# Performance work log

Measured on AMD Instinct MI355X. Metric: run time of the kernel, lower is better.

Reference implementation:

```python
import jax, jax.numpy as jnp
import numpy as np

ALPHA = 0.2  # leaky relu negative slope (LinearNet default)


def _init_linear(key, fan_in, fan_out):
    kw, kb = jax.random.split(key)
    lim = 1.0 / np.sqrt(fan_in)
    W = jax.random.uniform(kw, (fan_in, fan_out), jnp.float32, -lim, lim)
    b = jax.random.uniform(kb, (fan_out,), jnp.float32, -lim, lim)
    return W, b


def setup_inputs() -> dict:
    key = jax.random.key(0)
    keys = jax.random.split(key, 8)
    B, N, F = 8, 512, 32
    x = jax.random.normal(keys[0], (B, N, F), jnp.float32)
    # fe: [2F=64 -> 64 -> 64 -> 64], all layers leaky-relu (final_linear=False)
    fe_W0, fe_b0 = _init_linear(keys[1], 2 * F, 64)
    fe_W1, fe_b1 = _init_linear(keys[2], 64, 64)
    fe_W2, fe_b2 = _init_linear(keys[3], 64, 64)
    # fn: [64 + F = 96 -> 128 -> 128 -> 32], last layer linear (final_linear=True)
    fn_W0, fn_b0 = _init_linear(keys[4], 64 + F, 128)
    fn_W1, fn_b1 = _init_linear(keys[5], 128, 128)
    fn_W2, fn_b2 = _init_linear(keys[6], 128, 32)
    return {
        "x": x,
        "fe_W0": fe_W0, "fe_b0": fe_b0,
        "fe_W1": fe_W1, "fe_b1": fe_b1,
        "fe_W2": fe_W2, "fe_b2": fe_b2,
        "fn_W0": fn_W0, "fn_b0": fn_b0,
        "fn_W1": fn_W1, "fn_b1": fn_b1,
        "fn_W2": fn_W2, "fn_b2": fn_b2,
    }


def reference(x, fe_W0, fe_b0, fe_W1, fe_b1, fe_W2, fe_b2,
              fn_W0, fn_b0, fn_W1, fn_b1, fn_W2, fn_b2):
    B, N, F = x.shape
    # all-pairs edge inputs: A[b,i,j] = concat(x[b,i], x[b,j])  (x1=repeat rows, x2=tile)
    xi = jnp.broadcast_to(x[:, :, None, :], (B, N, N, F))
    xj = jnp.broadcast_to(x[:, None, :, :], (B, N, N, F))
    A = jnp.concatenate([xi, xj], axis=-1)  # [B, N, N, 2F]
    # edge MLP fe: leaky relu after every layer (final_linear=False)
    for W, b in ((fe_W0, fe_b0), (fe_W1, fe_b1), (fe_W2, fe_b2)):
        A = jax.nn.leaky_relu(A @ W + b, negative_slope=ALPHA)
    # sum aggregation over the sender axis j
    agg = jnp.sum(A, axis=2)  # [B, N, K]
    h = jnp.concatenate([agg, x], axis=-1)  # [B, N, K + F]
    # node MLP fn: leaky relu on hidden layers, final layer linear
    h = jax.nn.leaky_relu(h @ fn_W0 + fn_b0, negative_slope=ALPHA)
    h = jax.nn.leaky_relu(h @ fn_W1 + fn_b1, negative_slope=ALPHA)
    out = h @ fn_W2 + fn_b2  # [B, N, output_node_size]
    return out
```

## Files before the change

### kernel.cpp

```cpp
#include <hip/hip_runtime.h>
#include <hip/hip_bf16.h>

#define ALPHA 0.2f
static __device__ __forceinline__ float lrel(float x) { return fmaxf(x, ALPHA * x); }

typedef __attribute__((ext_vector_type(8))) short bf16x8;
typedef __attribute__((ext_vector_type(4))) float f32x4;

union FragU { bf16x8 v; unsigned int u[4]; uint4 q; };

static __device__ __forceinline__ unsigned int pk2(float a, float b) {
    unsigned int r;
    asm("v_cvt_pk_bf16_f32 %0, %1, %2" : "=v"(r) : "v"(a), "v"(b));
    return r;
}
static __device__ __forceinline__ unsigned int cvl2(float a, float b) {
    return pk2(lrel(a), lrel(b));
}
static __device__ __forceinline__ void addabs(float& a, float x) {
    asm("v_add_f32 %0, %0, |%1|" : "+v"(a) : "v"(x));
}
static __device__ __forceinline__ unsigned short f2bf(float x) {
    union { float f; unsigned int u; } c;
    c.f = x;
    unsigned int r = c.u + 0x7FFFu + ((c.u >> 16) & 1u);
    return (unsigned short)(r >> 16);
}
static __device__ __forceinline__ int pi64(int s) {
    return 32 * ((s >> 4) >> 1) + 8 * ((s >> 2) & 3) + 4 * ((s >> 4) & 1) + (s & 3);
}

__global__ __launch_bounds__(256) void k_uv(
    const float* __restrict__ x, const float* __restrict__ W0, const float* __restrict__ b0,
    const float* __restrict__ W1, const float* __restrict__ W2,
    float* __restrict__ Upi, unsigned short* __restrict__ xbf, unsigned int* __restrict__ WF)
{
    if (blockIdx.x == 1024) {
        const int t = threadIdx.x;
        const int l = t & 63, part = t >> 6;
        const int lo = l & 15, g = l >> 4;
        for (int ff = part; ff < 20; ff += 4) {
            unsigned int o[4];
            if (ff < 4) {
                const int nf = ff;
                const int pc = 32 * (nf >> 1) + 8 * (lo >> 2) + 4 * (nf & 1) + (lo & 3);
#pragma unroll
                for (int uq = 0; uq < 4; ++uq) {
                    const int k0 = 8 * g + 2 * uq;
                    o[uq] = pk2(W0[(32 + k0) * 64 + pc], W0[(33 + k0) * 64 + pc]);
                }
            } else if (ff < 12) {
                const int s = (ff - 4) >> 2, nf = (ff - 4) & 3;
                const int pc = 32 * (nf >> 1) + 8 * (lo >> 2) + 4 * (nf & 1) + (lo & 3);
#pragma unroll
                for (int uq = 0; uq < 4; ++uq) {
                    const int k0 = 32 * s + 8 * g + 2 * uq;
                    o[uq] = pk2(W1[k0 * 64 + pc], W1[(k0 + 1) * 64 + pc]);
                }
            } else {
                const int s = (ff - 12) >> 2, nf = (ff - 12) & 3;
                const int c2 = 16 * nf + lo;
#pragma unroll
                for (int uq = 0; uq < 4; ++uq) {
                    const int k0 = 32 * s + 8 * g + 2 * uq;
                    o[uq] = pk2(W2[k0 * 64 + c2], W2[(k0 + 1) * 64 + c2]);
                }
            }
            *(uint4*)(WF + (ff * 64 + l) * 4) = make_uint4(o[0], o[1], o[2], o[3]);
        }
        return;
    }
    const int idx = blockIdx.x * 256 + threadIdx.x;
    const int n = idx >> 6;
    const int slot = idx & 63;
    const int f = pi64(slot);
    const float* xr = x + n * 32;
    float u = b0[f];
#pragma unroll
    for (int i = 0; i < 32; ++i) u += xr[i] * W0[i * 64 + f];
    Upi[idx] = u;
    if (slot < 32) xbf[n * 32 + slot] = f2bf(xr[slot]);
}

__global__ __launch_bounds__(256, 2) void k_edge(
    const float* __restrict__ Upi, const unsigned short* __restrict__ xbf,
    const unsigned int* __restrict__ WF,
    const float* __restrict__ b1, const float* __restrict__ b2,
    float* __restrict__ AGG)
{
    __shared__ uint4 wlds[1024];
    const int tid = threadIdx.x;
    const int w = tid >> 6, l = tid & 63;
    const int lo = l & 15, g = l >> 4;
    const int bid = blockIdx.x;
    const int b = bid >> 7, ig = bid & 127;
    const int node = b * 512 + ig * 4 + w;

    for (int idx = tid; idx < 1024; idx += 256)
        wlds[idx] = ((const uint4*)WF)[256 + idx];

    FragU w0f[4];
    const uint4* wp = (const uint4*)WF;
#pragma unroll
    for (int nf = 0; nf < 4; ++nf) w0f[nf].q = wp[nf * 64 + l];

    f32x4 u0f[4], b1f[4], b2f[4];
#pragma unroll
    for (int nf = 0; nf < 4; ++nf) {
        const float4 t0 = *(const float4*)(Upi + node * 64 + nf * 16 + 4 * g);
        u0f[nf] = (f32x4){t0.x, t0.y, t0.z, t0.w};
        const float4 t1 = *(const float4*)(b1 + 32 * (nf >> 1) + 8 * g + 4 * (nf & 1));
        const float4 t2 = *(const float4*)(b2 + 16 * nf + 4 * g);
        b1f[nf] = (f32x4){t1.x, t1.y, t1.z, t1.w};
        b2f[nf] = (f32x4){t2.x, t2.y, t2.z, t2.w};
    }

    const unsigned short* xb = xbf + b * 512 * 32;

    FragU xjB, xjN;
    xjB.q = *(const uint4*)(xb + lo * 32 + 8 * g);
    xjN.q = *(const uint4*)(xb + (16 + lo) * 32 + 8 * g);

    __syncthreads();

    f32x4 acc0c[4];
#pragma unroll
    for (int nf = 0; nf < 4; ++nf)
        acc0c[nf] = __builtin_amdgcn_mfma_f32_16x16x32_bf16(w0f[nf].v, xjB.v, u0f[nf], 0, 0, 0);
    xjB = xjN;

    f32x4 acc2p[4];
#pragma unroll
    for (int nf = 0; nf < 4; ++nf) { f32x4 z = {0.f, 0.f, 0.f, 0.f}; acc2p[nf] = z; }

    float aggL[4][4], aggA[4][4];
#pragma unroll
    for (int nf = 0; nf < 4; ++nf)
#pragma unroll
        for (int r = 0; r < 4; ++r) { aggL[nf][r] = 0.f; aggA[nf][r] = 0.f; }

#pragma unroll 2
    for (int k = 0; k < 32; ++k) {
        int widx = 0;
        asm volatile("" : "+v"(widx));

        const int jn = ((k + 2) & 31) * 16;
        FragU xjn;
        xjn.q = *(const uint4*)(xb + (jn + lo) * 32 + 8 * g);

        f32x4 acc0n[4];
#pragma unroll
        for (int nf = 0; nf < 4; ++nf)
            acc0n[nf] = __builtin_amdgcn_mfma_f32_16x16x32_bf16(w0f[nf].v, xjB.v, u0f[nf], 0, 0, 0);

        FragU q0, q1;
        q0.u[0] = cvl2(acc0c[0][0], acc0c[0][1]);
        q0.u[1] = cvl2(acc0c[0][2], acc0c[0][3]);
        q0.u[2] = cvl2(acc0c[1][0], acc0c[1][1]);
        q0.u[3] = cvl2(acc0c[1][2], acc0c[1][3]);
        q1.u[0] = cvl2(acc0c[2][0], acc0c[2][1]);
        q1.u[1] = cvl2(acc0c[2][2], acc0c[2][3]);
        q1.u[2] = cvl2(acc0c[3][0], acc0c[3][1]);
        q1.u[3] = cvl2(acc0c[3][2], acc0c[3][3]);

        f32x4 acc1[4];
#pragma unroll
        for (int nf = 0; nf < 4; ++nf) {
            FragU wa, wb;
            wa.q = wlds[widx + nf * 64 + l];
            wb.q = wlds[widx + (4 + nf) * 64 + l];
            acc1[nf] = __builtin_amdgcn_mfma_f32_16x16x32_bf16(wa.v, q0.v, b1f[nf], 0, 0, 0);
            acc1[nf] = __builtin_amdgcn_mfma_f32_16x16x32_bf16(wb.v, q1.v, acc1[nf], 0, 0, 0);
        }

#pragma unroll
        for (int nf = 0; nf < 4; ++nf)
#pragma unroll
            for (int r = 0; r < 4; ++r) {
                aggL[nf][r] += acc2p[nf][r];
                addabs(aggA[nf][r], acc2p[nf][r]);
            }

        FragU p0, p1;
        p0.u[0] = cvl2(acc1[0][0], acc1[0][1]);
        p0.u[1] = cvl2(acc1[0][2], acc1[0][3]);
        p0.u[2] = cvl2(acc1[1][0], acc1[1][1]);
        p0.u[3] = cvl2(acc1[1][2], acc1[1][3]);
        p1.u[0] = cvl2(acc1[2][0], acc1[2][1]);
        p1.u[1] = cvl2(acc1[2][2], acc1[2][3]);
        p1.u[2] = cvl2(acc1[3][0], acc1[3][1]);
        p1.u[3] = cvl2(acc1[3][2], acc1[3][3]);

#pragma unroll
        for (int nf = 0; nf < 4; ++nf) {
            FragU wa, wb;
            wa.q = wlds[widx + (8 + nf) * 64 + l];
            wb.q = wlds[widx + (12 + nf) * 64 + l];
            acc2p[nf] = __builtin_amdgcn_mfma_f32_16x16x32_bf16(wa.v, p0.v, b2f[nf], 0, 0, 0);
            acc2p[nf] = __builtin_amdgcn_mfma_f32_16x16x32_bf16(wb.v, p1.v, acc2p[nf], 0, 0, 0);
        }

#pragma unroll
        for (int nf = 0; nf < 4; ++nf) acc0c[nf] = acc0n[nf];
        xjB = xjn;
    }

#pragma unroll
    for (int nf = 0; nf < 4; ++nf)
#pragma unroll
        for (int r = 0; r < 4; ++r) {
            aggL[nf][r] += acc2p[nf][r];
            addabs(aggA[nf][r], acc2p[nf][r]);
        }

#pragma unroll
    for (int nf = 0; nf < 4; ++nf)
#pragma unroll
        for (int r = 0; r < 4; ++r) {
            float v = 0.6f * aggL[nf][r] + 0.4f * aggA[nf][r];
            v += __shfl_xor(v, 1);
            v += __shfl_xor(v, 2);
            v += __shfl_xor(v, 4);
            v += __shfl_xor(v, 8);
            aggL[nf][r] = v;
        }
    if (lo == 0) {
#pragma unroll
        for (int nf = 0; nf < 4; ++nf) {
            float4 o = {aggL[nf][0], aggL[nf][1], aggL[nf][2], aggL[nf][3]};
            *(float4*)(AGG + node * 64 + 16 * nf + 4 * g) = o;
        }
    }
}

__global__ __launch_bounds__(256) void k_fn(
    const float* __restrict__ AGG, const float* __restrict__ x,
    const float* __restrict__ W0, const float* __restrict__ b0,
    const float* __restrict__ W1, const float* __restrict__ b1,
    const float* __restrict__ W2, const float* __restrict__ b2,
    float* __restrict__ out)
{
    __shared__ float in96T[96][8];
    __shared__ float h1T[128][8];
    __shared__ float h2T[128][8];
    const int t = threadIdx.x;
    const int half = t >> 7, f = t & 127;
    const int node0 = blockIdx.x * 8;

    for (int idx = t; idx < 768; idx += 256) {
        int nn = idx & 7, k = idx >> 3;
        in96T[k][nn] = (k < 64) ? AGG[(node0 + nn) * 64 + k]
                                : x[(node0 + nn) * 32 + (k - 64)];
    }
    __syncthreads();

    {
        float a0 = b0[f], a1 = a0, a2 = a0, a3 = a0;
#pragma unroll 4
        for (int k = 0; k < 96; ++k) {
            const float4 iv = *(const float4*)(&in96T[k][4 * half]);
            const float wv = W0[k * 128 + f];
            a0 += iv.x * wv; a1 += iv.y * wv; a2 += iv.z * wv; a3 += iv.w * wv;
        }
        float4 o = {lrel(a0), lrel(a1), lrel(a2), lrel(a3)};
        *(float4*)(&h1T[f][4 * half]) = o;
    }
    __syncthreads();

    {
        float a0 = b1[f], a1 = a0, a2 = a0, a3 = a0;
#pragma unroll 4
        for (int k = 0; k < 128; ++k) {
            const float4 iv = *(const float4*)(&h1T[k][4 * half]);
            const float wv = W1[k * 128 + f];
            a0 += iv.x * wv; a1 += iv.y * wv; a2 += iv.z * wv; a3 += iv.w * wv;
        }
        float4 o = {lrel(a0), lrel(a1), lrel(a2), lrel(a3)};
        *(float4*)(&h2T[f][4 * half]) = o;
    }
    __syncthreads();

    {
        const int nn = t >> 5, fo = t & 31;
        float a = b2[fo];
#pragma unroll 4
        for (int k = 0; k < 128; ++k) a += h2T[k][nn] * W2[k * 32 + fo];
        out[(node0 + nn) * 32 + fo] = a;
    }
}

extern "C" void kernel_launch(void* const* d_in, const int* in_sizes, int n_in,
                              void* d_out, int out_size, void* d_ws, size_t ws_size,
                              hipStream_t stream)
{
    const float* x    = (const float*)d_in[0];
    const float* feW0 = (const float*)d_in[1];
    const float* feb0 = (const float*)d_in[2];
    const float* feW1 = (const float*)d_in[3];
    const float* feb1 = (const float*)d_in[4];
    const float* feW2 = (const float*)d_in[5];
    const float* feb2 = (const float*)d_in[6];
    const float* fnW0 = (const float*)d_in[7];
    const float* fnb0 = (const float*)d_in[8];
    const float* fnW1 = (const float*)d_in[9];
    const float* fnb1 = (const float*)d_in[10];
    const float* fnW2 = (const float*)d_in[11];
    const float* fnb2 = (const float*)d_in[12];
    float* out = (float*)d_out;

    float* Upi = (float*)d_ws;
    float* AGG = Upi + 262144;
    unsigned short* xbf = (unsigned short*)(AGG + 262144);
    unsigned int* WF = (unsigned int*)(xbf + 131072);

    hipLaunchKernelGGL(k_uv,   dim3(1025), dim3(256), 0, stream, x, feW0, feb0, feW1, feW2, Upi, xbf, WF);
    hipLaunchKernelGGL(k_edge, dim3(1024), dim3(256), 0, stream, Upi, xbf, WF, feb1, feb2, AGG);
    hipLaunchKernelGGL(k_fn,   dim3(512),  dim3(256), 0, stream, AGG, x, fnW0, fnb0, fnW1, fnb1, fnW2, fnb2, out);
}
```

Baseline: 74.54 us.

## Software-pipeline the three edge-MLP layers across consecutive sender tiles

```diff
diff --git a/kernel.cpp b/kernel.cpp
--- a/kernel.cpp
+++ b/kernel.cpp
@@ -16,9 +16,6 @@
 }
 static __device__ __forceinline__ unsigned int cvl2(float a, float b) {
     return pk2(lrel(a), lrel(b));
-}
-static __device__ __forceinline__ void addabs(float& a, float x) {
-    asm("v_add_f32 %0, %0, |%1|" : "+v"(a) : "v"(x));
 }
 static __device__ __forceinline__ unsigned short f2bf(float x) {
     union { float f; unsigned int u; } c;
@@ -117,30 +114,30 @@
 
     const unsigned short* xb = xbf + b * 512 * 32;
 
-    FragU xjB, xjN;
-    xjB.q = *(const uint4*)(xb + lo * 32 + 8 * g);
-    xjN.q = *(const uint4*)(xb + (16 + lo) * 32 + 8 * g);
+    FragU xjT0, xjB;
+    xjT0.q = *(const uint4*)(xb + lo * 32 + 8 * g);
+    xjB.q  = *(const uint4*)(xb + (16 + lo) * 32 + 8 * g);
 
     __syncthreads();
 
-    f32x4 acc0c[4];
+    f32x4 acc0p[4], acc1p[4], acc2p[4];
 #pragma unroll
     for (int nf = 0; nf < 4; ++nf)
-        acc0c[nf] = __builtin_amdgcn_mfma_f32_16x16x32_bf16(w0f[nf].v, xjB.v, u0f[nf], 0, 0, 0);
-    xjB = xjN;
-
-    f32x4 acc2p[4];
-#pragma unroll
-    for (int nf = 0; nf < 4; ++nf) { f32x4 z = {0.f, 0.f, 0.f, 0.f}; acc2p[nf] = z; }
-
-    float aggL[4][4], aggA[4][4];
+        acc0p[nf] = __builtin_amdgcn_mfma_f32_16x16x32_bf16(w0f[nf].v, xjT0.v, u0f[nf], 0, 0, 0);
+#pragma unroll
+    for (int nf = 0; nf < 4; ++nf) {
+        f32x4 z = {0.f, 0.f, 0.f, 0.f};
+        acc1p[nf] = z; acc2p[nf] = z;
+    }
+
+    float aggL[4][4];
 #pragma unroll
     for (int nf = 0; nf < 4; ++nf)
 #pragma unroll
-        for (int r = 0; r < 4; ++r) { aggL[nf][r] = 0.f; aggA[nf][r] = 0.f; }
+        for (int r = 0; r < 4; ++r) aggL[nf][r] = 0.f;
 
 #pragma unroll 2
-    for (int k = 0; k < 32; ++k) {
+    for (int k = 0; k < 34; ++k) {
         int widx = 0;
         asm volatile("" : "+v"(widx));
 
@@ -148,60 +145,64 @@
         FragU xjn;
         xjn.q = *(const uint4*)(xb + (jn + lo) * 32 + 8 * g);
 
+        FragU q0, q1;
+        q0.u[0] = cvl2(acc0p[0][0], acc0p[0][1]);
+        q0.u[1] = cvl2(acc0p[0][2], acc0p[0][3]);
+        q0.u[2] = cvl2(acc0p[1][0], acc0p[1][1]);
+        q0.u[3] = cvl2(acc0p[1][2], acc0p[1][3]);
+        q1.u[0] = cvl2(acc0p[2][0], acc0p[2][1]);
+        q1.u[1] = cvl2(acc0p[2][2], acc0p[2][3]);
+        q1.u[2] = cvl2(acc0p[3][0], acc0p[3][1]);
+        q1.u[3] = cvl2(acc0p[3][2], acc0p[3][3]);
+
         f32x4 acc0n[4];
 #pragma unroll
         for (int nf = 0; nf < 4; ++nf)
             acc0n[nf] = __builtin_amdgcn_mfma_f32_16x16x32_bf16(w0f[nf].v, xjB.v, u0f[nf], 0, 0, 0);
 
-        FragU q0, q1;
-        q0.u[0] = cvl2(acc0c[0][0], acc0c[0][1]);
-        q0.u[1] = cvl2(acc0c[0][2], acc0c[0][3]);
-        q0.u[2] = cvl2(acc0c[1][0], acc0c[1][1]);
-        q0.u[3] = cvl2(acc0c[1][2], acc0c[1][3]);
-        q1.u[0] = cvl2(acc0c[2][0], acc0c[2][1]);
-        q1.u[1] = cvl2(acc0c[2][2], acc0c[2][3]);
-        q1.u[2] = cvl2(acc0c[3][0], acc0c[3][1]);
-        q1.u[3] = cvl2(acc0c[3][2], acc0c[3][3]);
-
-        f32x4 acc1[4];
+        FragU p0, p1;
+        p0.u[0] = cvl2(acc1p[0][0], acc1p[0][1]);
+        p0.u[1] = cvl2(acc1p[0][2], acc1p[0][3]);
+        p0.u[2] = cvl2(acc1p[1][0], acc1p[1][1]);
+        p0.u[3] = cvl2(acc1p[1][2], acc1p[1][3]);
+        p1.u[0] = cvl2(acc1p[2][0], acc1p[2][1]);
+        p1.u[1] = cvl2(acc1p[2][2], acc1p[2][3]);
+        p1.u[2] = cvl2(acc1p[3][0], acc1p[3][1]);
+        p1.u[3] = cvl2(acc1p[3][2], acc1p[3][3]);
+
+        f32x4 acc1n[4];
 #pragma unroll
         for (int nf = 0; nf < 4; ++nf) {
             FragU wa, wb;
             wa.q = wlds[widx + nf * 64 + l];
             wb.q = wlds[widx + (4 + nf) * 64 + l];
-            acc1[nf] = __builtin_amdgcn_mfma_f32_16x16x32_bf16(wa.v, q0.v, b1f[nf], 0, 0, 0);
-            acc1[nf] = __builtin_amdgcn_mfma_f32_16x16x32_bf16(wb.v, q1.v, acc1[nf], 0, 0, 0);
-        }
-
-#pragma unroll
-        for (int nf = 0; nf < 4; ++nf)
-#pragma unroll
-            for (int r = 0; r < 4; ++r) {
-                aggL[nf][r] += acc2p[nf][r];
-                addabs(aggA[nf][r], acc2p[nf][r]);
-            }
-
-        FragU p0, p1;
-        p0.u[0] = cvl2(acc1[0][0], acc1[0][1]);
-        p0.u[1] = cvl2(acc1[0][2], acc1[0][3]);
-        p0.u[2] = cvl2(acc1[1][0], acc1[1][1]);
-        p0.u[3] = cvl2(acc1[1][2], acc1[1][3]);
-        p1.u[0] = cvl2(acc1[2][0], acc1[2][1]);
-        p1.u[1] = cvl2(acc1[2][2], acc1[2][3]);
-        p1.u[2] = cvl2(acc1[3][0], acc1[3][1]);
-        p1.u[3] = cvl2(acc1[3][2], acc1[3][3]);
-
+            acc1n[nf] = __builtin_amdgcn_mfma_f32_16x16x32_bf16(wa.v, q0.v, b1f[nf], 0, 0, 0);
+            acc1n[nf] = __builtin_amdgcn_mfma_f32_16x16x32_bf16(wb.v, q1.v, acc1n[nf], 0, 0, 0);
+        }
+
+        if (k >= 2) {
+#pragma unroll
+            for (int nf = 0; nf < 4; ++nf)
+#pragma unroll
+                for (int r = 0; r < 4; ++r) aggL[nf][r] += lrel(acc2p[nf][r]);
+        }
+
+        f32x4 acc2n[4];
 #pragma unroll
         for (int nf = 0; nf < 4; ++nf) {
             FragU wa, wb;
             wa.q = wlds[widx + (8 + nf) * 64 + l];
             wb.q = wlds[widx + (12 + nf) * 64 + l];
-            acc2p[nf] = __builtin_amdgcn_mfma_f32_16x16x32_bf16(wa.v, p0.v, b2f[nf], 0, 0, 0);
-            acc2p[nf] = __builtin_amdgcn_mfma_f32_16x16x32_bf16(wb.v, p1.v, acc2p[nf], 0, 0, 0);
-        }
-
-#pragma unroll
-        for (int nf = 0; nf < 4; ++nf) acc0c[nf] = acc0n[nf];
+            acc2n[nf] = __builtin_amdgcn_mfma_f32_16x16x32_bf16(wa.v, p0.v, b2f[nf], 0, 0, 0);
+            acc2n[nf] = __builtin_amdgcn_mfma_f32_16x16x32_bf16(wb.v, p1.v, acc2n[nf], 0, 0, 0);
+        }
+
+#pragma unroll
+        for (int nf = 0; nf < 4; ++nf) {
+            acc0p[nf] = acc0n[nf];
+            acc1p[nf] = acc1n[nf];
+            acc2p[nf] = acc2n[nf];
+        }
         xjB = xjn;
     }
 
@@ -209,15 +210,7 @@
     for (int nf = 0; nf < 4; ++nf)
 #pragma unroll
         for (int r = 0; r < 4; ++r) {
-            aggL[nf][r] += acc2p[nf][r];
-            addabs(aggA[nf][r], acc2p[nf][r]);
-        }
-
-#pragma unroll
-    for (int nf = 0; nf < 4; ++nf)
-#pragma unroll
-        for (int r = 0; r < 4; ++r) {
-            float v = 0.6f * aggL[nf][r] + 0.4f * aggA[nf][r];
+            float v = aggL[nf][r];
             v += __shfl_xor(v, 1);
             v += __shfl_xor(v, 2);
             v += __shfl_xor(v, 4);
```

New measurement: 85.27 us. 1.14x slower.

## Fold leaky-relu into aggregation, raise occupancy to 3, prioritize MFMA issue

Applied to the files above, without the earlier changes.

```diff
diff --git a/kernel.cpp b/kernel.cpp
--- a/kernel.cpp
+++ b/kernel.cpp
@@ -16,9 +16,6 @@
 }
 static __device__ __forceinline__ unsigned int cvl2(float a, float b) {
     return pk2(lrel(a), lrel(b));
-}
-static __device__ __forceinline__ void addabs(float& a, float x) {
-    asm("v_add_f32 %0, %0, |%1|" : "+v"(a) : "v"(x));
 }
 static __device__ __forceinline__ unsigned short f2bf(float x) {
     union { float f; unsigned int u; } c;
@@ -82,7 +79,7 @@
     if (slot < 32) xbf[n * 32 + slot] = f2bf(xr[slot]);
 }
 
-__global__ __launch_bounds__(256, 2) void k_edge(
+__global__ __launch_bounds__(256, 3) void k_edge(
     const float* __restrict__ Upi, const unsigned short* __restrict__ xbf,
     const unsigned int* __restrict__ WF,
     const float* __restrict__ b1, const float* __restrict__ b2,
@@ -117,27 +114,26 @@
 
     const unsigned short* xb = xbf + b * 512 * 32;
 
-    FragU xjB, xjN;
-    xjB.q = *(const uint4*)(xb + lo * 32 + 8 * g);
-    xjN.q = *(const uint4*)(xb + (16 + lo) * 32 + 8 * g);
+    FragU xjT0, xjB;
+    xjT0.q = *(const uint4*)(xb + lo * 32 + 8 * g);
+    xjB.q  = *(const uint4*)(xb + (16 + lo) * 32 + 8 * g);
 
     __syncthreads();
 
     f32x4 acc0c[4];
 #pragma unroll
     for (int nf = 0; nf < 4; ++nf)
-        acc0c[nf] = __builtin_amdgcn_mfma_f32_16x16x32_bf16(w0f[nf].v, xjB.v, u0f[nf], 0, 0, 0);
-    xjB = xjN;
+        acc0c[nf] = __builtin_amdgcn_mfma_f32_16x16x32_bf16(w0f[nf].v, xjT0.v, u0f[nf], 0, 0, 0);
 
     f32x4 acc2p[4];
 #pragma unroll
     for (int nf = 0; nf < 4; ++nf) { f32x4 z = {0.f, 0.f, 0.f, 0.f}; acc2p[nf] = z; }
 
-    float aggL[4][4], aggA[4][4];
+    float aggL[4][4];
 #pragma unroll
     for (int nf = 0; nf < 4; ++nf)
 #pragma unroll
-        for (int r = 0; r < 4; ++r) { aggL[nf][r] = 0.f; aggA[nf][r] = 0.f; }
+        for (int r = 0; r < 4; ++r) aggL[nf][r] = 0.f;
 
 #pragma unroll 2
     for (int k = 0; k < 32; ++k) {
@@ -148,10 +144,12 @@
         FragU xjn;
         xjn.q = *(const uint4*)(xb + (jn + lo) * 32 + 8 * g);
 
+        __builtin_amdgcn_s_setprio(1);
         f32x4 acc0n[4];
 #pragma unroll
         for (int nf = 0; nf < 4; ++nf)
             acc0n[nf] = __builtin_amdgcn_mfma_f32_16x16x32_bf16(w0f[nf].v, xjB.v, u0f[nf], 0, 0, 0);
+        __builtin_amdgcn_s_setprio(0);
 
         FragU q0, q1;
         q0.u[0] = cvl2(acc0c[0][0], acc0c[0][1]);
@@ -163,6 +161,7 @@
         q1.u[2] = cvl2(acc0c[3][0], acc0c[3][1]);
         q1.u[3] = cvl2(acc0c[3][2], acc0c[3][3]);
 
+        __builtin_amdgcn_s_setprio(1);
         f32x4 acc1[4];
 #pragma unroll
         for (int nf = 0; nf < 4; ++nf) {
@@ -172,14 +171,12 @@
             acc1[nf] = __builtin_amdgcn_mfma_f32_16x16x32_bf16(wa.v, q0.v, b1f[nf], 0, 0, 0);
             acc1[nf] = __builtin_amdgcn_mfma_f32_16x16x32_bf16(wb.v, q1.v, acc1[nf], 0, 0, 0);
         }
+        __builtin_amdgcn_s_setprio(0);
 
 #pragma unroll
         for (int nf = 0; nf < 4; ++nf)
 #pragma unroll
-            for (int r = 0; r < 4; ++r) {
-                aggL[nf][r] += acc2p[nf][r];
-                addabs(aggA[nf][r], acc2p[nf][r]);
-            }
+            for (int r = 0; r < 4; ++r) aggL[nf][r] += lrel(acc2p[nf][r]);
 
         FragU p0, p1;
         p0.u[0] = cvl2(acc1[0][0], acc1[0][1]);
@@ -191,6 +188,7 @@
         p1.u[2] = cvl2(acc1[3][0], acc1[3][1]);
         p1.u[3] = cvl2(acc1[3][2], acc1[3][3]);
 
+        __builtin_amdgcn_s_setprio(1);
 #pragma unroll
         for (int nf = 0; nf < 4; ++nf) {
             FragU wa, wb;
@@ -199,6 +197,7 @@
             acc2p[nf] = __builtin_amdgcn_mfma_f32_16x16x32_bf16(wa.v, p0.v, b2f[nf], 0, 0, 0);
             acc2p[nf] = __builtin_amdgcn_mfma_f32_16x16x32_bf16(wb.v, p1.v, acc2p[nf], 0, 0, 0);
         }
+        __builtin_amdgcn_s_setprio(0);
 
 #pragma unroll
         for (int nf = 0; nf < 4; ++nf) acc0c[nf] = acc0n[nf];
@@ -208,16 +207,13 @@
 #pragma unroll
     for (int nf = 0; nf < 4; ++nf)
 #pragma unroll
+        for (int r = 0; r < 4; ++r) aggL[nf][r] += lrel(acc2p[nf][r]);
+
+#pragma unroll
+    for (int nf = 0; nf < 4; ++nf)
+#pragma unroll
         for (int r = 0; r < 4; ++r) {
-            aggL[nf][r] += acc2p[nf][r];
-            addabs(aggA[nf][r], acc2p[nf][r]);
-        }
-
-#pragma unroll
-    for (int nf = 0; nf < 4; ++nf)
-#pragma unroll
-        for (int r = 0; r < 4; ++r) {
-            float v = 0.6f * aggL[nf][r] + 0.4f * aggA[nf][r];
+            float v = aggL[nf][r];
             v += __shfl_xor(v, 1);
             v += __shfl_xor(v, 2);
             v += __shfl_xor(v, 4);
```

Result: slower. 81.27 us (+9.0%).
